# Optimization experiments

Hardware: AMD Instinct MI355X
Metric: run time of the kernel (lower is better)

The kernel has to match this reference:

```python
import jax, jax.numpy as jnp
import numpy as np

EPS_ALPHA = 1e-7
EPS_STEP = 1e-6


def setup_inputs() -> dict:
    key = jax.random.key(0)
    k1, k2, k3 = jax.random.split(key, 3)
    B, T, D = 32, 1024, 512
    x = jax.random.normal(k1, (B, T, D), dtype=jnp.float32)
    # Linear(in_dim, 1) params (sigmoid-gain init approximated with small normal)
    W = jax.random.normal(k2, (D, 1), dtype=jnp.float32) * (1.0 / np.sqrt(D))
    b = jnp.zeros((1,), dtype=jnp.float32)
    return {"x": x, "W": W, "b": b, "r": 1, "num_steps": 1024}


def reference(x, W, b, r, num_steps):
    # x: [B, T, D]; r is unused (as in the original forward)
    B, T, D = x.shape
    speeds = jax.nn.sigmoid(jnp.einsum('btd,do->bto', x, W) + b)  # [B, T, 1]
    sp = speeds[:, :, 0]  # [B, T]

    # alpha0 = [1, 1e-7, 1e-7, ...]
    alpha0 = jnp.concatenate(
        [jnp.ones((B, 1), x.dtype), jnp.full((B, T - 1), EPS_ALPHA, x.dtype)], axis=1)

    def step(alpha, _):
        # u = alpha . speeds  -> [B, 1]
        u = jnp.sum(alpha * sp, axis=1, keepdims=True)
        sq = 1.7 - jnp.abs(u - 0.5)  # 1 + 0.7 - |u-0.5|
        shifted = jnp.pad(alpha[:, :-1], ((0, 0), (1, 0)))  # forward shift
        a = ((1.0 - u) * alpha + u * shifted + EPS_STEP) ** sq
        a = a / jnp.sum(a, axis=1, keepdims=True)
        return a, a

    _, alphas = jax.lax.scan(step, alpha0, None, length=num_steps)  # [S, B, T]
    alphas = jnp.transpose(alphas, (1, 0, 2))  # [B, S, T]
    contexts = jnp.einsum('bst,btd->bsd', alphas, x)  # [B, S, D]
    return contexts, alphas
```

## Files before the change

### kernel.cpp

```cpp
#include <hip/hip_runtime.h>
#include <hip/hip_bf16.h>

#define NB 32
#define NT 1024
#define ND 512
#define NS 1024

#define CTX_ELEMS (32u * 1024u * 512u)
#define SP_SCRATCH_OFF (CTX_ELEMS - 32u*1024u)

__device__ __forceinline__ float vlog2(float x) {
    float r; asm("v_log_f32 %0, %1" : "=v"(r) : "v"(x)); return r;
}
__device__ __forceinline__ float vexp2(float x) {
    float r; asm("v_exp_f32 %0, %1" : "=v"(r) : "v"(x)); return r;
}
__device__ __forceinline__ float vrcp(float x) {
    float r; asm("v_rcp_f32 %0, %1" : "=v"(r) : "v"(x)); return r;
}

template<int ctrl, int rm, int bm, bool bc>
__device__ __forceinline__ float dppadd(float x) {
    int y = __builtin_amdgcn_update_dpp(0, __float_as_int(x), ctrl, rm, bm, bc);
    return x + __int_as_float(y);
}
__device__ __forceinline__ float reduce63(float x) {
    x = dppadd<0x111, 0xf, 0xf, true >(x);
    x = dppadd<0x112, 0xf, 0xf, true >(x);
    x = dppadd<0x114, 0xf, 0xf, true >(x);
    x = dppadd<0x118, 0xf, 0xf, true >(x);
    x = dppadd<0x142, 0xa, 0xf, false>(x);
    x = dppadd<0x143, 0xc, 0xf, false>(x);
    return x;
}
__device__ __forceinline__ float wave_shr1(float x) {
    int y = __builtin_amdgcn_update_dpp(0, __float_as_int(x), 0x138, 0xf, 0xf, true);
    return __int_as_float(y);
}

__device__ __forceinline__ void lds_barrier() {
    asm volatile("s_waitcnt lgkmcnt(0)" ::: "memory");
    __builtin_amdgcn_s_barrier();
    asm volatile("" ::: "memory");
}

__global__ __launch_bounds__(256) void sp_kernel(const float* __restrict__ x,
                                                 const float* __restrict__ W,
                                                 const float* __restrict__ bias,
                                                 float* __restrict__ sp)
{
    const int lane = threadIdx.x & 63;
    const int wid  = threadIdx.x >> 6;
    const int row  = blockIdx.x * 4 + wid;
    const float4* xr = reinterpret_cast<const float4*>(x + (size_t)row * ND) + lane * 2;
    const float4* wr = reinterpret_cast<const float4*>(W) + lane * 2;
    float4 xa = xr[0], xb = xr[1];
    float4 wa = wr[0], wb = wr[1];
    float d = xa.x*wa.x + xa.y*wa.y + xa.z*wa.z + xa.w*wa.w
            + xb.x*wb.x + xb.y*wb.y + xb.z*wb.z + xb.w*wb.w;
    #pragma unroll
    for (int m = 1; m < 64; m <<= 1) d += __shfl_xor(d, m);
    if (lane == 0) {
        float z = d + bias[0];
        float e = vexp2(-z * 1.442695040888963f);
        sp[row] = 1.0f / (1.0f + e);
    }
}

__global__ __launch_bounds__(512) void scan_kernel(const float* __restrict__ sp,
                                                   float* __restrict__ alphas)
{
    const int b    = blockIdx.x;
    const int tx   = threadIdx.x;
    const int lane = tx & 63;
    const int wid  = tx >> 6;

    __shared__ __align__(16) float r1[2][8];
    __shared__ __align__(16) float r2[2][8];
    __shared__ __align__(16) float rb[2][8];

    float spv[2], raw[2];
    {
        float2 v = *reinterpret_cast<const float2*>(sp + (size_t)b * NT + tx * 2);
        spv[0] = v.x; spv[1] = v.y;
    }
    raw[0] = 1e-7f; raw[1] = 1e-7f;
    if (tx == 0) raw[0] = 1.0f;
    float carry = (wid == 0) ? 0.0f : 1e-7f;

    {
        float q = fmaf(raw[0], spv[0], raw[1] * spv[1]);
        q = reduce63(q);
        if (lane == 63) r2[1][wid] = q;
    }
    lds_barrier();
    float u;
    {
        float4 a = *reinterpret_cast<const float4*>(&r2[1][0]);
        float4 c = *reinterpret_cast<const float4*>(&r2[1][4]);
        u = ((a.x + a.y) + (a.z + a.w)) + ((c.x + c.y) + (c.z + c.w));
    }
    float inv = 1.0f;

    float* outp = alphas + (size_t)b * NS * NT + tx * 2;

    for (int s = 0; s < NS; ++s) {
        const int p = s & 1;
        const float sq = 1.7f - fabsf(u - 0.5f);
        const float c1 = (1.0f - u) * inv;
        const float c0 = u * inv;

        float prev = wave_shr1(raw[1]);
        float sh0  = (lane == 0) ? carry : prev;

        float an0 = vexp2(sq * vlog2(fmaf(c1, raw[0], fmaf(c0, sh0,    1e-6f))));
        float an1 = vexp2(sq * vlog2(fmaf(c1, raw[1], fmaf(c0, raw[0], 1e-6f))));

        float p1 = an0 + an1;
        float p2 = fmaf(an0, spv[0], an1 * spv[1]);
        p1 = reduce63(p1);
        p2 = reduce63(p2);
        if (lane == 63) { r1[p][wid] = p1; r2[p][wid] = p2; rb[p][wid] = an1; }
        lds_barrier();

        float4 a = *reinterpret_cast<const float4*>(&r1[p][0]);
        float4 bq = *reinterpret_cast<const float4*>(&r1[p][4]);
        float4 c = *reinterpret_cast<const float4*>(&r2[p][0]);
        float4 d = *reinterpret_cast<const float4*>(&r2[p][4]);
        float bc = rb[p][(wid == 0) ? 0 : (wid - 1)];
        carry = (wid == 0) ? 0.0f : bc;

        float t1 = ((a.x + a.y) + (a.z + a.w)) + ((bq.x + bq.y) + (bq.z + bq.w));
        float t2 = ((c.x + c.y) + (c.z + c.w)) + ((d.x + d.y) + (d.z + d.w));
        inv = vrcp(t1);
        u   = t2 * inv;

        float2 o;
        o.x = an0 * inv; o.y = an1 * inv;
        *reinterpret_cast<float2*>(outp + (size_t)s * NT) = o;

        raw[0] = an0; raw[1] = an1;
    }
}

typedef __bf16 bf16x8 __attribute__((ext_vector_type(8)));
typedef float  f32x4  __attribute__((ext_vector_type(4)));

#define BM 256
#define BN 256
#define BK 32
#define LDP 40

__global__ __launch_bounds__(512, 2) void gemm_kernel(const float* __restrict__ alphas,
                                                      const float* __restrict__ x,
                                                      float* __restrict__ contexts)
{
    __shared__ __align__(16) __bf16 As[BM * LDP];
    __shared__ __align__(16) __bf16 Xs[BN * LDP];

    const int bid  = blockIdx.x;
    const int low3 = bid & 7;
    const int slot = bid >> 3;
    const int nb   = slot & 1;
    const int pair = (slot >> 1) * 8 + low3;
    const int b    = pair >> 2;
    const int sbi  = pair & 3;
    const int s0 = sbi * BM;
    const int n0 = nb * BN;

    const int tx = threadIdx.x;
    const int lane = tx & 63;
    const int wid  = tx >> 6;
    const int wm = wid >> 2;
    const int wn = wid & 3;
    const int lr = lane & 15;
    const int lk = (lane >> 4) * 8;

    f32x4 acc[8][4];
    #pragma unroll
    for (int i = 0; i < 8; ++i)
        #pragma unroll
        for (int j = 0; j < 4; ++j) acc[i][j] = (f32x4){0.f, 0.f, 0.f, 0.f};

    const int arow = tx >> 1;
    const int akb  = (tx & 1) * 16;
    const int xk0 = tx >> 6;
    const int xn4 = (tx & 63) * 4;

    const float* ap = alphas + ((size_t)b * NS + s0 + arow) * NT + akb;
    const float* xp = x + ((size_t)b * NT + xk0) * ND + n0 + xn4;

    float4 va0 = reinterpret_cast<const float4*>(ap)[0];
    float4 va1 = reinterpret_cast<const float4*>(ap)[1];
    float4 va2 = reinterpret_cast<const float4*>(ap)[2];
    float4 va3 = reinterpret_cast<const float4*>(ap)[3];
    float4 vx0 = *reinterpret_cast<const float4*>(xp + 0 * 8 * ND);
    float4 vx1 = *reinterpret_cast<const float4*>(xp + 1 * 8 * ND);
    float4 vx2 = *reinterpret_cast<const float4*>(xp + 2 * 8 * ND);
    float4 vx3 = *reinterpret_cast<const float4*>(xp + 3 * 8 * ND);
    ap += BK;
    xp += (size_t)BK * ND;

    for (int k0 = 0; k0 < NT; k0 += BK) {
        {
            bf16x8 w0, w1;
            w0[0]=(__bf16)va0.x; w0[1]=(__bf16)va0.y; w0[2]=(__bf16)va0.z; w0[3]=(__bf16)va0.w;
            w0[4]=(__bf16)va1.x; w0[5]=(__bf16)va1.y; w0[6]=(__bf16)va1.z; w0[7]=(__bf16)va1.w;
            w1[0]=(__bf16)va2.x; w1[1]=(__bf16)va2.y; w1[2]=(__bf16)va2.z; w1[3]=(__bf16)va2.w;
            w1[4]=(__bf16)va3.x; w1[5]=(__bf16)va3.y; w1[6]=(__bf16)va3.z; w1[7]=(__bf16)va3.w;
            *reinterpret_cast<bf16x8*>(&As[arow * LDP + akb])     = w0;
            *reinterpret_cast<bf16x8*>(&As[arow * LDP + akb + 8]) = w1;
            Xs[(xn4+0)*LDP + xk0]      = (__bf16)vx0.x;
            Xs[(xn4+1)*LDP + xk0]      = (__bf16)vx0.y;
            Xs[(xn4+2)*LDP + xk0]      = (__bf16)vx0.z;
            Xs[(xn4+3)*LDP + xk0]      = (__bf16)vx0.w;
            Xs[(xn4+0)*LDP + xk0 + 8]  = (__bf16)vx1.x;
            Xs[(xn4+1)*LDP + xk0 + 8]  = (__bf16)vx1.y;
            Xs[(xn4+2)*LDP + xk0 + 8]  = (__bf16)vx1.z;
            Xs[(xn4+3)*LDP + xk0 + 8]  = (__bf16)vx1.w;
            Xs[(xn4+0)*LDP + xk0 + 16] = (__bf16)vx2.x;
            Xs[(xn4+1)*LDP + xk0 + 16] = (__bf16)vx2.y;
            Xs[(xn4+2)*LDP + xk0 + 16] = (__bf16)vx2.z;
            Xs[(xn4+3)*LDP + xk0 + 16] = (__bf16)vx2.w;
            Xs[(xn4+0)*LDP + xk0 + 24] = (__bf16)vx3.x;
            Xs[(xn4+1)*LDP + xk0 + 24] = (__bf16)vx3.y;
            Xs[(xn4+2)*LDP + xk0 + 24] = (__bf16)vx3.z;
            Xs[(xn4+3)*LDP + xk0 + 24] = (__bf16)vx3.w;
        }
        if (k0 + BK < NT) {
            va0 = reinterpret_cast<const float4*>(ap)[0];
            va1 = reinterpret_cast<const float4*>(ap)[1];
            va2 = reinterpret_cast<const float4*>(ap)[2];
            va3 = reinterpret_cast<const float4*>(ap)[3];
            vx0 = *reinterpret_cast<const float4*>(xp + 0 * 8 * ND);
            vx1 = *reinterpret_cast<const float4*>(xp + 1 * 8 * ND);
            vx2 = *reinterpret_cast<const float4*>(xp + 2 * 8 * ND);
            vx3 = *reinterpret_cast<const float4*>(xp + 3 * 8 * ND);
            ap += BK;
            xp += (size_t)BK * ND;
        }
        lds_barrier();

        bf16x8 av[8], bv[4];
        #pragma unroll
        for (int j = 0; j < 4; ++j)
            bv[j] = *reinterpret_cast<const bf16x8*>(&Xs[(wn*64 + j*16 + lr) * LDP + lk]);
        #pragma unroll
        for (int i = 0; i < 8; ++i)
            av[i] = *reinterpret_cast<const bf16x8*>(&As[(wm*128 + i*16 + lr) * LDP + lk]);
        #pragma unroll
        for (int i = 0; i < 8; ++i)
            #pragma unroll
            for (int j = 0; j < 4; ++j)
                acc[i][j] = __builtin_amdgcn_mfma_f32_16x16x32_bf16(av[i], bv[j], acc[i][j], 0, 0, 0);
        lds_barrier();
    }

    const int ccol = lr;
    const int crow = (lane >> 4) * 4;
    #pragma unroll
    for (int i = 0; i < 8; ++i) {
        #pragma unroll
        for (int j = 0; j < 4; ++j) {
            int col = n0 + wn*64 + j*16 + ccol;
            int rw  = s0 + wm*128 + i*16 + crow;
            #pragma unroll
            for (int r = 0; r < 4; ++r)
                contexts[((size_t)b * NS + rw + r) * ND + col] = acc[i][j][r];
        }
    }
}

extern "C" void kernel_launch(void* const* d_in, const int* in_sizes, int n_in,
                              void* d_out, int out_size, void* d_ws, size_t ws_size,
                              hipStream_t stream) {
    const float* x    = (const float*)d_in[0];
    const float* W    = (const float*)d_in[1];
    const float* bias = (const float*)d_in[2];
    float* contexts = (float*)d_out;
    float* alphas   = (float*)d_out + CTX_ELEMS;
    float* sp       = (float*)d_out + SP_SCRATCH_OFF;

    sp_kernel<<<dim3(NB * NT / 4), dim3(256), 0, stream>>>(x, W, bias, sp);
    scan_kernel<<<dim3(NB), dim3(512), 0, stream>>>(sp, alphas);
    gemm_kernel<<<dim3(256), dim3(512), 0, stream>>>(alphas, x, contexts);
}
```

Baseline: 477.6 us.

## Shrink scan block to 4 waves with 4 elements per thread and packed exchange

The sequential scan kernel now runs 256 threads per batch row, each handling 4 alpha elements instead of 2. This halves the number of waves taking part in each per-step barrier and packs the cross-wave partial sums and carry into a single float4 slot. The step algebra is also rewritten so the previous step's normalisation is folded into precomputed coefficients (cA, tt2, inv2). The output store is deferred by one step so it overlaps the barrier. The trade-off is more serial exp/log work per thread on the 1024-step critical path and slightly different floating-point rounding.

```diff
diff --git a/kernel.cpp b/kernel.cpp
--- a/kernel.cpp
+++ b/kernel.cpp
@@ -67,7 +67,7 @@
     }
 }
 
-__global__ __launch_bounds__(512) void scan_kernel(const float* __restrict__ sp,
+__global__ __launch_bounds__(256) void scan_kernel(const float* __restrict__ sp,
                                                    float* __restrict__ alphas)
 {
     const int b    = blockIdx.x;
@@ -75,72 +75,111 @@
     const int lane = tx & 63;
     const int wid  = tx >> 6;
 
-    __shared__ __align__(16) float r1[2][8];
-    __shared__ __align__(16) float r2[2][8];
-    __shared__ __align__(16) float rb[2][8];
-
-    float spv[2], raw[2];
-    {
-        float2 v = *reinterpret_cast<const float2*>(sp + (size_t)b * NT + tx * 2);
-        spv[0] = v.x; spv[1] = v.y;
-    }
-    raw[0] = 1e-7f; raw[1] = 1e-7f;
+    __shared__ __align__(16) float4 xch[2][4];
+
+    float spv[4], raw[4], an[4], o[4];
+    {
+        float4 v = *reinterpret_cast<const float4*>(sp + (size_t)b * NT + tx * 4);
+        spv[0] = v.x; spv[1] = v.y; spv[2] = v.z; spv[3] = v.w;
+    }
+    #pragma unroll
+    for (int j = 0; j < 4; ++j) raw[j] = 1e-7f;
     if (tx == 0) raw[0] = 1.0f;
     float carry = (wid == 0) ? 0.0f : 1e-7f;
 
     {
-        float q = fmaf(raw[0], spv[0], raw[1] * spv[1]);
+        float q = fmaf(raw[0], spv[0], fmaf(raw[1], spv[1], fmaf(raw[2], spv[2], raw[3]*spv[3])));
         q = reduce63(q);
-        if (lane == 63) r2[1][wid] = q;
+        if (lane == 63) xch[1][wid] = make_float4(q, 0.f, 0.f, 0.f);
     }
     lds_barrier();
-    float u;
-    {
-        float4 a = *reinterpret_cast<const float4*>(&r2[1][0]);
-        float4 c = *reinterpret_cast<const float4*>(&r2[1][4]);
-        u = ((a.x + a.y) + (a.z + a.w)) + ((c.x + c.y) + (c.z + c.w));
-    }
-    float inv = 1.0f;
-
-    float* outp = alphas + (size_t)b * NS * NT + tx * 2;
-
-    for (int s = 0; s < NS; ++s) {
-        const int p = s & 1;
-        const float sq = 1.7f - fabsf(u - 0.5f);
-        const float c1 = (1.0f - u) * inv;
-        const float c0 = u * inv;
-
-        float prev = wave_shr1(raw[1]);
+    float u, inv, inv2, sq, cA, tt2;
+    {
+        float4 x0 = xch[1][0], x1 = xch[1][1], x2 = xch[1][2], x3 = xch[1][3];
+        u = (x0.x + x1.x) + (x2.x + x3.x);
+    }
+
+    float* outp = alphas + (size_t)b * NS * NT + tx * 4;
+
+    {
+        sq = 1.7f - fabsf(u - 0.5f);
+        const float c1 = 1.0f - u;
+        const float c0 = u;
+        float prev = wave_shr1(raw[3]);
         float sh0  = (lane == 0) ? carry : prev;
-
-        float an0 = vexp2(sq * vlog2(fmaf(c1, raw[0], fmaf(c0, sh0,    1e-6f))));
-        float an1 = vexp2(sq * vlog2(fmaf(c1, raw[1], fmaf(c0, raw[0], 1e-6f))));
-
-        float p1 = an0 + an1;
-        float p2 = fmaf(an0, spv[0], an1 * spv[1]);
+        an[0] = vexp2(sq * vlog2(fmaf(c1, raw[0], fmaf(c0, sh0,    1e-6f))));
+        an[1] = vexp2(sq * vlog2(fmaf(c1, raw[1], fmaf(c0, raw[0], 1e-6f))));
+        an[2] = vexp2(sq * vlog2(fmaf(c1, raw[2], fmaf(c0, raw[1], 1e-6f))));
+        an[3] = vexp2(sq * vlog2(fmaf(c1, raw[3], fmaf(c0, raw[2], 1e-6f))));
+        float p1 = (an[0] + an[1]) + (an[2] + an[3]);
+        float p2 = fmaf(an[0], spv[0], an[1]*spv[1]) + fmaf(an[2], spv[2], an[3]*spv[3]);
         p1 = reduce63(p1);
         p2 = reduce63(p2);
-        if (lane == 63) { r1[p][wid] = p1; r2[p][wid] = p2; rb[p][wid] = an1; }
+        if (lane == 63) xch[0][wid] = make_float4(p1, p2, an[3], 0.f);
         lds_barrier();
-
-        float4 a = *reinterpret_cast<const float4*>(&r1[p][0]);
-        float4 bq = *reinterpret_cast<const float4*>(&r1[p][4]);
-        float4 c = *reinterpret_cast<const float4*>(&r2[p][0]);
-        float4 d = *reinterpret_cast<const float4*>(&r2[p][4]);
-        float bc = rb[p][(wid == 0) ? 0 : (wid - 1)];
-        carry = (wid == 0) ? 0.0f : bc;
-
-        float t1 = ((a.x + a.y) + (a.z + a.w)) + ((bq.x + bq.y) + (bq.z + bq.w));
-        float t2 = ((c.x + c.y) + (c.z + c.w)) + ((d.x + d.y) + (d.z + d.w));
-        inv = vrcp(t1);
-        u   = t2 * inv;
-
-        float2 o;
-        o.x = an0 * inv; o.y = an1 * inv;
-        *reinterpret_cast<float2*>(outp + (size_t)s * NT) = o;
-
-        raw[0] = an0; raw[1] = an1;
-    }
+        float4 x0 = xch[0][0], x1 = xch[0][1], x2 = xch[0][2], x3 = xch[0][3];
+        float bc = (wid == 1) ? x0.z : (wid == 2) ? x1.z : (wid == 3) ? x2.z : 0.0f;
+        carry = bc;
+        float t1 = (x0.x + x1.x) + (x2.x + x3.x);
+        float t2 = (x0.y + x1.y) + (x2.y + x3.y);
+        inv  = vrcp(t1);
+        inv2 = inv * inv;
+        u    = t2 * inv;
+        sq   = 1.7f - fabsf(u - 0.5f);
+        cA   = t1 - t2;
+        tt2  = t2;
+        #pragma unroll
+        for (int j = 0; j < 4; ++j) { o[j] = an[j] * inv; raw[j] = an[j]; }
+    }
+
+#define STEPB(SLOT)                                                                     \
+    do {                                                                                \
+        float prev = wave_shr1(raw[3]);                                                 \
+        float sh0  = (lane == 0) ? carry : prev;                                        \
+        float w0 = fmaf(cA, raw[0], tt2 * sh0);                                         \
+        float w1 = fmaf(cA, raw[1], tt2 * raw[0]);                                      \
+        float w2 = fmaf(cA, raw[2], tt2 * raw[1]);                                      \
+        float w3 = fmaf(cA, raw[3], tt2 * raw[2]);                                      \
+        an[0] = vexp2(sq * vlog2(fmaf(w0, inv2, 1e-6f)));                               \
+        an[1] = vexp2(sq * vlog2(fmaf(w1, inv2, 1e-6f)));                               \
+        an[2] = vexp2(sq * vlog2(fmaf(w2, inv2, 1e-6f)));                               \
+        an[3] = vexp2(sq * vlog2(fmaf(w3, inv2, 1e-6f)));                               \
+        float p1 = (an[0] + an[1]) + (an[2] + an[3]);                                   \
+        float p2 = fmaf(an[0], spv[0], an[1]*spv[1]) + fmaf(an[2], spv[2], an[3]*spv[3]);\
+        p1 = reduce63(p1);                                                              \
+        p2 = reduce63(p2);                                                              \
+        if (lane == 63) xch[SLOT][wid] = make_float4(p1, p2, an[3], 0.f);               \
+        {                           \
+            float4 ov; ov.x = o[0]; ov.y = o[1]; ov.z = o[2]; ov.w = o[3];              \
+            *reinterpret_cast<float4*>(outp) = ov;                                      \
+            outp += NT;                                                                 \
+        }                                                                               \
+        lds_barrier();                                                                  \
+        float4 x0 = xch[SLOT][0], x1 = xch[SLOT][1], x2 = xch[SLOT][2], x3 = xch[SLOT][3];\
+        float bc = (wid == 1) ? x0.z : (wid == 2) ? x1.z : (wid == 3) ? x2.z : 0.0f;    \
+        carry = bc;                                                                     \
+        float t1 = (x0.x + x1.x) + (x2.x + x3.x);                                       \
+        float t2 = (x0.y + x1.y) + (x2.y + x3.y);                                       \
+        inv  = vrcp(t1);                                                                \
+        inv2 = inv * inv;                                                               \
+        u    = t2 * inv;                                                                \
+        sq   = 1.7f - fabsf(u - 0.5f);                                                  \
+        cA   = t1 - t2;                                                                 \
+        tt2  = t2;                                                                      \
+        _Pragma("unroll")                                                               \
+        for (int j = 0; j < 4; ++j) { o[j] = an[j] * inv; raw[j] = an[j]; }             \
+    } while (0)
+
+    for (int s = 1; s <= 1021; s += 2) {
+        STEPB(1);
+        STEPB(0);
+    }
+    STEPB(1);
+    {
+        float4 ov; ov.x = o[0]; ov.y = o[1]; ov.z = o[2]; ov.w = o[3];
+        *reinterpret_cast<float4*>(outp) = ov;
+    }
+#undef STEPB
 }
 
 typedef __bf16 bf16x8 __attribute__((ext_vector_type(8)));
@@ -282,6 +321,6 @@
     float* sp       = (float*)d_out + SP_SCRATCH_OFF;
 
     sp_kernel<<<dim3(NB * NT / 4), dim3(256), 0, stream>>>(x, W, bias, sp);
-    scan_kernel<<<dim3(NB), dim3(512), 0, stream>>>(sp, alphas);
+    scan_kernel<<<dim3(NB), dim3(256), 0, stream>>>(sp, alphas);
     gemm_kernel<<<dim3(256), dim3(512), 0, stream>>>(alphas, x, contexts);
 }
```

Measured after the change: 426.6 us. -10.7%, faster.
